# Kernel tuning notes

Hardware: AMD Instinct MI355X
Metric: run time of the kernel (lower is better)

## Reference

```python
import jax, jax.numpy as jnp
import numpy as np

N_NODES = 50000
N_EDGES = 1600000
NODE_DIM = 16
EDGE_DIM = 16
PIPE_F = 4
HID = 64
L = 3


def _lin(k, fan_in, fan_out):
    kw, kb = jax.random.split(k)
    bound = 1.0 / np.sqrt(fan_in)
    w = jax.random.uniform(kw, (fan_in, fan_out), jnp.float32, -bound, bound)
    b = jax.random.uniform(kb, (fan_out,), jnp.float32, -bound, bound)
    return w, b


def setup_inputs() -> dict:
    key = jax.random.key(0)
    ks = jax.random.split(key, 16)
    leak_area = jax.random.normal(ks[0], (N_NODES, 1), jnp.float32)
    pipe_attrs = jax.random.normal(ks[1], (N_EDGES, PIPE_F), jnp.float32)
    edge_index = jax.random.randint(ks[2], (2, N_EDGES), 0, N_NODES, jnp.int32)
    node_embed_w, node_embed_b = _lin(ks[3], 1, NODE_DIM)
    edge_embed_w, edge_embed_b = _lin(ks[4], PIPE_F, EDGE_DIM)
    # per-layer MLP params, stacked along leading layer axis
    ew1, eb1, ew2, eb2, nw1, nb1, nw2, nb2 = [], [], [], [], [], [], [], []
    for l in range(L):
        kl = jax.random.fold_in(ks[5], l)
        k1, k2, k3, k4 = jax.random.split(kl, 4)
        w, b = _lin(k1, 2 * NODE_DIM + EDGE_DIM, HID); ew1.append(w); eb1.append(b)
        w, b = _lin(k2, HID, EDGE_DIM); ew2.append(w); eb2.append(b)
        w, b = _lin(k3, NODE_DIM + EDGE_DIM, HID); nw1.append(w); nb1.append(b)
        w, b = _lin(k4, HID, NODE_DIM); nw2.append(w); nb2.append(b)
    final_node_w, final_node_b = _lin(ks[6], NODE_DIM, 1)
    final_edge_w, final_edge_b = _lin(ks[7], EDGE_DIM, 1)
    return {
        "leak_area": leak_area,
        "pipe_attrs": pipe_attrs,
        "edge_index": edge_index,
        "node_embed_w": node_embed_w, "node_embed_b": node_embed_b,
        "edge_embed_w": edge_embed_w, "edge_embed_b": edge_embed_b,
        "edge_mlp_w1": jnp.stack(ew1), "edge_mlp_b1": jnp.stack(eb1),
        "edge_mlp_w2": jnp.stack(ew2), "edge_mlp_b2": jnp.stack(eb2),
        "node_mlp_w1": jnp.stack(nw1), "node_mlp_b1": jnp.stack(nb1),
        "node_mlp_w2": jnp.stack(nw2), "node_mlp_b2": jnp.stack(nb2),
        "final_node_w": final_node_w, "final_node_b": final_node_b,
        "final_edge_w": final_edge_w, "final_edge_b": final_edge_b,
    }


def reference(leak_area, pipe_attrs, edge_index,
              node_embed_w, node_embed_b, edge_embed_w, edge_embed_b,
              edge_mlp_w1, edge_mlp_b1, edge_mlp_w2, edge_mlp_b2,
              node_mlp_w1, node_mlp_b1, node_mlp_w2, node_mlp_b2,
              final_node_w, final_node_b, final_edge_w, final_edge_b):
    x = leak_area @ node_embed_w + node_embed_b          # [N, node_dim]
    e = pipe_attrs @ edge_embed_w + edge_embed_b          # [E, edge_dim]
    src = edge_index[0]  # x_j (source, PyG default flow source_to_target)
    dst = edge_index[1]  # x_i (target); aggregation index
    n = x.shape[0]
    num_layers = edge_mlp_w1.shape[0]
    ones = jnp.ones((src.shape[0], 1), x.dtype)
    deg = jax.ops.segment_sum(ones, dst, num_segments=n)  # [N,1]
    inv_deg = 1.0 / jnp.maximum(deg, 1.0)
    for l in range(num_layers):
        # message: small MLP on [x_i, x_j, e] per edge
        m_in = jnp.concatenate([x[dst], x[src], e], axis=-1)       # [E, 2d+de]
        h = jax.nn.relu(m_in @ edge_mlp_w1[l] + edge_mlp_b1[l])    # [E, 64]
        msg = h @ edge_mlp_w2[l] + edge_mlp_b2[l]                  # [E, de]
        # mean-aggregate to target nodes
        aggr = jax.ops.segment_sum(msg, dst, num_segments=n) * inv_deg  # [N, de]
        # node update MLP
        u_in = jnp.concatenate([x, aggr], axis=-1)                 # [N, d+de]
        x = jax.nn.relu(u_in @ node_mlp_w1[l] + node_mlp_b1[l]) @ node_mlp_w2[l] + node_mlp_b2[l]
    H = (x @ final_node_w + final_node_b)[:, 0]   # [N]
    q = (e @ final_edge_w + final_edge_b)[:, 0]   # [E]
    return H, q
```

## Files before the change

kernel.cpp:

```cpp
#include <hip/hip_runtime.h>
#include <hip/hip_bf16.h>

#define NN 50000
#define NE 1600000
#define NB 391
#define CBLK 392
#define EPB 4096

typedef __attribute__((ext_vector_type(8))) short bf16x8;
typedef __attribute__((ext_vector_type(4))) float f32x4;

#define B_HAG   0
#define B_QW    (B_HAG + NN*64*4)
#define B_NF    (B_QW + 32)
#define B_W1B   (B_NF + 3*8*64*8*2)
#define B_XB0   (B_W1B + 3*8*64*8*2)
#define B_XB1   (B_XB0 + NN*16*2)
#define B_EPK   (B_XB1 + NN*16*2)
#define B_OFF   (B_EPK + NE*16)
#define B_BCNT  (B_OFF + (NN+1)*4)
#define B_BASE  (B_BCNT + CBLK*NB*4)
#define B_END   (B_BASE + (NB+1)*4)

static __device__ __forceinline__ unsigned short f2bf(float f) {
    union { __hip_bfloat16 h; unsigned short u; } cv;
    cv.h = __float2bfloat16(f);
    return cv.u;
}
static __device__ __forceinline__ unsigned pk2(float a, float b) {
    unsigned r;
    asm("v_cvt_pk_bf16_f32 %0, %1, %2" : "=v"(r) : "v"(a), "v"(b));
    return r;
}
static __device__ __forceinline__ float bf2f(unsigned short u) {
    return __uint_as_float((unsigned)u << 16);
}
static __device__ __forceinline__ bf16x8 mk8(unsigned a, unsigned b, unsigned c, unsigned d) {
    union { bf16x8 v; uint4 u; } cv;
    cv.u = make_uint4(a, b, c, d);
    return cv.v;
}

__global__ void prep_kernel(const float* __restrict__ ew1, const float* __restrict__ eb1,
                            const float* __restrict__ nw1, const float* __restrict__ ew2,
                            const float* __restrict__ nw2,
                            const float* __restrict__ eeW, const float* __restrict__ eeB,
                            const float* __restrict__ few, const float* __restrict__ feb,
                            unsigned short* __restrict__ w1b, unsigned short* __restrict__ nf,
                            float* __restrict__ qw)
{
    int t0 = blockIdx.x * blockDim.x + threadIdx.x;
    int stride = gridDim.x * blockDim.x;
    for (int idx = t0; idx < 3 * 8 * 64 * 8; idx += stride) {
        int l = idx >> 12;
        int r = idx & 4095;
        int f = r >> 9;
        int lane = (r >> 3) & 63;
        int e = r & 7;
        int col = lane & 15;
        int krow = ((lane >> 4) << 3) + e;
        {
            int tt = f >> 1, s = f & 1;
            int k = krow + (s << 5);
            int j = (tt << 4) + col;
            float v = 0.f;
            if (k < 32) {
                v = ew1[l * 3072 + k * 64 + j];
            } else if (k < 36) {
                int f2 = k - 32;
                float acc = 0.f;
                for (int m = 0; m < 16; m++) acc += eeW[f2 * 16 + m] * ew1[l * 3072 + (32 + m) * 64 + j];
                v = acc;
            } else if (k == 36) {
                float acc = eb1[l * 64 + j];
                for (int m = 0; m < 16; m++) acc += eeB[m] * ew1[l * 3072 + (32 + m) * 64 + j];
                v = acc;
            }
            w1b[idx] = f2bf(v);
        }
        {
            float v;
            if (f < 2)      v = ew2[l * 1024 + (f * 32 + krow) * 16 + col];
            else if (f < 6) v = nw1[l * 2048 + krow * 64 + (f - 2) * 16 + col];
            else            v = nw2[l * 1024 + ((f - 6) * 32 + krow) * 16 + col];
            nf[idx] = f2bf(v);
        }
    }
    if (t0 < 4) {
        float s = 0.f;
        for (int k = 0; k < 16; k++) s += eeW[t0 * 16 + k] * few[k];
        qw[t0] = s;
    } else if (t0 == 4) {
        float s = feb[0];
        for (int k = 0; k < 16; k++) s += eeB[k] * few[k];
        qw[4] = s;
    }
}

__global__ __launch_bounds__(256) void node_init_kernel(
    const float* __restrict__ leak, const float* __restrict__ nw, const float* __restrict__ nb,
    unsigned short* __restrict__ xb0, float* __restrict__ hag)
{
    int n = blockIdx.x * blockDim.x + threadIdx.x;
    if (n >= NN) return;
    float la = leak[n];
    float v[16];
    #pragma unroll
    for (int i = 0; i < 16; i++) v[i] = la * nw[i] + nb[i];
    unsigned pk[8];
    #pragma unroll
    for (int i = 0; i < 8; i++) pk[i] = pk2(v[2 * i], v[2 * i + 1]);
    uint4* xo = reinterpret_cast<uint4*>(xb0 + n * 16);
    xo[0] = make_uint4(pk[0], pk[1], pk[2], pk[3]);
    xo[1] = make_uint4(pk[4], pk[5], pk[6], pk[7]);
    float4 z = {0.f, 0.f, 0.f, 0.f};
    float4* hp = reinterpret_cast<float4*>(hag + n * 64);
    #pragma unroll
    for (int j = 0; j < 16; j++) hp[j] = z;
}

__global__ __launch_bounds__(1024) void bucket_count_kernel(
    const int* __restrict__ dst, int* __restrict__ bcnt)
{
    __shared__ int hist[NB];
    int t = threadIdx.x;
    for (int i = t; i < NB; i += 1024) hist[i] = 0;
    __syncthreads();
    int base = blockIdx.x * EPB;
    #pragma unroll
    for (int i = 0; i < 4; i++) {
        int idx = base + i * 1024 + t;
        if (idx < NE) atomicAdd(&hist[dst[idx] >> 7], 1);
    }
    __syncthreads();
    for (int i = t; i < NB; i += 1024) bcnt[blockIdx.x * NB + i] = hist[i];
}

__global__ __launch_bounds__(512) void bucket_scan_kernel(
    int* __restrict__ bcnt, int* __restrict__ gbase)
{
    __shared__ int sm[512];
    int t = threadIdx.x;
    int tot = 0;
    if (t < NB)
        for (int blk = 0; blk < CBLK; blk++) tot += bcnt[blk * NB + t];
    sm[t] = tot;
    __syncthreads();
    for (int o = 1; o < 512; o <<= 1) {
        int v = (t >= o) ? sm[t - o] : 0;
        __syncthreads();
        sm[t] += v;
        __syncthreads();
    }
    int excl = sm[t] - tot;
    if (t < NB) {
        gbase[t] = excl;
        int run = excl;
        for (int blk = 0; blk < CBLK; blk++) {
            int c = bcnt[blk * NB + t];
            bcnt[blk * NB + t] = run;
            run += c;
        }
    }
    if (t == 0) gbase[NB] = NE;
}

__global__ __launch_bounds__(1024) void bucket_scatter_kernel(
    const int* __restrict__ ei, const float* __restrict__ pa,
    const int* __restrict__ bcnt, const float* __restrict__ qw,
    float* __restrict__ qout, uint4* __restrict__ epk)
{
    __shared__ int hist[NB];
    int t = threadIdx.x;
    for (int i = t; i < NB; i += 1024) hist[i] = 0;
    __syncthreads();
    int base = blockIdx.x * EPB;
    #pragma unroll
    for (int i = 0; i < 4; i++) {
        int idx = base + i * 1024 + t;
        if (idx < NE) {
            int d = ei[NE + idx];
            int b = d >> 7;
            float4 p = reinterpret_cast<const float4*>(pa)[idx];
            qout[idx] = qw[4] + p.x * qw[0] + p.y * qw[1] + p.z * qw[2] + p.w * qw[3];
            int lr = atomicAdd(&hist[b], 1);
            int pos = bcnt[blockIdx.x * NB + b] + lr;
            uint4 v;
            v.x = (unsigned)ei[idx];
            v.y = (unsigned)d;
            v.z = pk2(p.x, p.y);
            v.w = pk2(p.z, p.w);
            epk[pos] = v;
        }
    }
}

__global__ __launch_bounds__(1024) void fine_sort_kernel(
    const int* __restrict__ gbase, uint4* __restrict__ epk, int* __restrict__ off)
{
    __shared__ int hist[128];
    __shared__ int fb[128];
    int t = threadIdx.x;
    int b = blockIdx.x;
    int S = gbase[b], E = gbase[b + 1];
    if (t < 128) hist[t] = 0;
    __syncthreads();

    uint4 r[12];
    int lr[12];
    #pragma unroll
    for (int i = 0; i < 12; i++) {
        int gi = S + i * 1024 + t;
        if (gi < E) {
            r[i] = epk[gi];
            lr[i] = atomicAdd(&hist[(int)(r[i].y & 127u)], 1);
        }
    }
    __syncthreads();
    if (t < 128) fb[t] = hist[t];
    __syncthreads();
    for (int o = 1; o < 128; o <<= 1) {
        int v = 0;
        if (t < 128 && t >= o) v = fb[t - o];
        __syncthreads();
        if (t < 128) fb[t] += v;
        __syncthreads();
    }
    int d0 = b << 7;
    if (t < 128 && d0 + t < NN) off[d0 + t] = S + fb[t] - hist[t];
    if (b == NB - 1 && t == 0) off[NN] = NE;
    __syncthreads();
    #pragma unroll
    for (int i = 0; i < 12; i++) {
        int gi = S + i * 1024 + t;
        if (gi < E) {
            int fd = (int)(r[i].y & 127u);
            int pos = S + (fb[fd] - hist[fd]) + lr[i];
            epk[pos] = r[i];
        }
    }
}

__global__ __launch_bounds__(256, 4) void edge_mfma_kernel(
    const unsigned short* __restrict__ xb,
    const uint4* __restrict__ epk,
    const int* __restrict__ off,
    const unsigned short* __restrict__ w1b,
    float* __restrict__ hag)
{
    __shared__ unsigned short hbuf[4][64 * 68];
    int tid = threadIdx.x;
    int lane = tid & 63;
    int wid = tid >> 6;
    int wave = blockIdx.x * 4 + wid;
    int base = wave * 64;
    if (base >= NE) return;
    int ar = lane & 15;
    int ap = lane >> 4;
    unsigned short* hb = &hbuf[wid][0];

    uint4 ev0 = epk[base + 0  + ar];
    uint4 ev1 = epk[base + 16 + ar];
    uint4 ev2 = epk[base + 32 + ar];
    uint4 ev3 = epk[base + 48 + ar];

    int r0 = (ap < 2) ? (int)ev0.y : (int)ev0.x;
    int r1 = (ap < 2) ? (int)ev1.y : (int)ev1.x;
    int r2 = (ap < 2) ? (int)ev2.y : (int)ev2.x;
    int r3 = (ap < 2) ? (int)ev3.y : (int)ev3.x;
    int half = (ap & 1) * 8;
    bf16x8 a00 = *reinterpret_cast<const bf16x8*>(xb + (size_t)r0 * 16 + half);
    bf16x8 a01 = *reinterpret_cast<const bf16x8*>(xb + (size_t)r1 * 16 + half);
    bf16x8 a02 = *reinterpret_cast<const bf16x8*>(xb + (size_t)r2 * 16 + half);
    bf16x8 a03 = *reinterpret_cast<const bf16x8*>(xb + (size_t)r3 * 16 + half);

    int d0 = __builtin_amdgcn_readfirstlane((int)ev0.y);

    bf16x8 Bf[8];
    const bf16x8* w1v = reinterpret_cast<const bf16x8*>(w1b);
    #pragma unroll
    for (int i = 0; i < 8; i++) Bf[i] = w1v[i * 64 + lane];

#define DO_TILE(EV, A0, TILE) do {                                             \
    bf16x8 a1 = (bf16x8)0;                                                     \
    if (ap == 0) {                                                             \
        a1[0] = (short)(EV.z & 0xffffu);                                       \
        a1[1] = (short)(EV.z >> 16);                                           \
        a1[2] = (short)(EV.w & 0xffffu);                                       \
        a1[3] = (short)(EV.w >> 16);                                           \
        a1[4] = (short)0x3f80;                                                 \
    }                                                                          \
    f32x4 C0 = {0.f, 0.f, 0.f, 0.f}, C1 = C0, C2 = C0, C3 = C0;                \
    C0 = __builtin_amdgcn_mfma_f32_16x16x32_bf16(A0, Bf[0], C0, 0, 0, 0);      \
    C0 = __builtin_amdgcn_mfma_f32_16x16x32_bf16(a1, Bf[1], C0, 0, 0, 0);      \
    C1 = __builtin_amdgcn_mfma_f32_16x16x32_bf16(A0, Bf[2], C1, 0, 0, 0);      \
    C1 = __builtin_amdgcn_mfma_f32_16x16x32_bf16(a1, Bf[3], C1, 0, 0, 0);      \
    C2 = __builtin_amdgcn_mfma_f32_16x16x32_bf16(A0, Bf[4], C2, 0, 0, 0);      \
    C2 = __builtin_amdgcn_mfma_f32_16x16x32_bf16(a1, Bf[5], C2, 0, 0, 0);      \
    C3 = __builtin_amdgcn_mfma_f32_16x16x32_bf16(A0, Bf[6], C3, 0, 0, 0);      \
    C3 = __builtin_amdgcn_mfma_f32_16x16x32_bf16(a1, Bf[7], C3, 0, 0, 0);      \
    int eoff = TILE * 16 + ap * 4;                                             \
    {                                                                          \
        unsigned lov = pk2(fmaxf(C0[0], 0.f), fmaxf(C0[1], 0.f));              \
        unsigned hiv = pk2(fmaxf(C0[2], 0.f), fmaxf(C0[3], 0.f));              \
        *reinterpret_cast<uint2*>(hb + (0 * 16 + ar) * 68 + eoff) = make_uint2(lov, hiv); \
    }                                                                          \
    {                                                                          \
        unsigned lov = pk2(fmaxf(C1[0], 0.f), fmaxf(C1[1], 0.f));              \
        unsigned hiv = pk2(fmaxf(C1[2], 0.f), fmaxf(C1[3], 0.f));              \
        *reinterpret_cast<uint2*>(hb + (1 * 16 + ar) * 68 + eoff) = make_uint2(lov, hiv); \
    }                                                                          \
    {                                                                          \
        unsigned lov = pk2(fmaxf(C2[0], 0.f), fmaxf(C2[1], 0.f));              \
        unsigned hiv = pk2(fmaxf(C2[2], 0.f), fmaxf(C2[3], 0.f));              \
        *reinterpret_cast<uint2*>(hb + (2 * 16 + ar) * 68 + eoff) = make_uint2(lov, hiv); \
    }                                                                          \
    {                                                                          \
        unsigned lov = pk2(fmaxf(C3[0], 0.f), fmaxf(C3[1], 0.f));              \
        unsigned hiv = pk2(fmaxf(C3[2], 0.f), fmaxf(C3[3], 0.f));              \
        *reinterpret_cast<uint2*>(hb + (3 * 16 + ar) * 68 + eoff) = make_uint2(lov, hiv); \
    }                                                                          \
} while (0)

    DO_TILE(ev0, a00, 0);
    DO_TILE(ev1, a01, 1);
    DO_TILE(ev2, a02, 2);
    DO_TILE(ev3, a03, 3);
#undef DO_TILE

    asm volatile("s_waitcnt lgkmcnt(0)" ::: "memory");
    __builtin_amdgcn_sched_barrier(0);

    int d = d0;
    int e = base;
    const int lim = base + 64;
    const unsigned short* hr = hb + lane * 68;
    while (e < lim) {
        int segend = off[d + 1];
        int eend = segend < lim ? segend : lim;
        float acc = 0.f;
        int i = e - base, iend = eend - base;
        for (; (i & 3) != 0 && i < iend; ++i) acc += bf2f(hr[i]);
        for (; i + 4 <= iend; i += 4) {
            uint2 u = *reinterpret_cast<const uint2*>(hr + i);
            acc += __uint_as_float(u.x << 16) + __uint_as_float(u.x & 0xffff0000u)
                 + __uint_as_float(u.y << 16) + __uint_as_float(u.y & 0xffff0000u);
        }
        for (; i < iend; ++i) acc += bf2f(hr[i]);
        unsafeAtomicAdd(&hag[(size_t)d * 64 + lane], acc);
        e = eend;
        if (segend <= lim) ++d;
    }
}

__global__ __launch_bounds__(256) void node_mfma_kernel(
    const unsigned short* __restrict__ xb, unsigned short* __restrict__ xbn,
    float* __restrict__ hag, const int* __restrict__ off,
    const unsigned short* __restrict__ nf,
    const float* __restrict__ eb2,
    const float* __restrict__ nb1, const float* __restrict__ nb2,
    const float* __restrict__ fnw, const float* __restrict__ fnb,
    float* __restrict__ Hout, int writeH)
{
    __shared__ unsigned short aggt[4][16 * 16];
    __shared__ unsigned short ht[4][16 * 64];
    __shared__ float ot[4][16 * 16];
    int tid = threadIdx.x;
    int lane = tid & 63;
    int wid = tid >> 6;
    int wave = blockIdx.x * 4 + wid;
    int n0 = wave * 16;
    if (n0 >= NN) return;
    int nr = lane & 15;
    int ap = lane >> 4;

    bf16x8 Bf[8];
    const bf16x8* nfv = reinterpret_cast<const bf16x8*>(nf);
    #pragma unroll
    for (int i = 0; i < 8; i++) Bf[i] = nfv[i * 64 + lane];

    float* hrow = hag + (size_t)(n0 + nr) * 64 + ap * 8;
    float4* h0p = reinterpret_cast<float4*>(hrow);
    float4* h1p = reinterpret_cast<float4*>(hrow + 32);
    float4 ha = h0p[0], hc = h0p[1];
    float4 he = h1p[0], hg = h1p[1];
    float4 z = {0.f, 0.f, 0.f, 0.f};
    h0p[0] = z; h0p[1] = z; h1p[0] = z; h1p[1] = z;
    bf16x8 agA0 = mk8(pk2(ha.x, ha.y), pk2(ha.z, ha.w), pk2(hc.x, hc.y), pk2(hc.z, hc.w));
    bf16x8 agA1 = mk8(pk2(he.x, he.y), pk2(he.z, he.w), pk2(hg.x, hg.y), pk2(hg.z, hg.w));
    f32x4 Cag = {0.f, 0.f, 0.f, 0.f};
    Cag = __builtin_amdgcn_mfma_f32_16x16x32_bf16(agA0, Bf[0], Cag, 0, 0, 0);
    Cag = __builtin_amdgcn_mfma_f32_16x16x32_bf16(agA1, Bf[1], Cag, 0, 0, 0);

    int bn = n0 + ap * 4;
    int o0 = off[bn], o1 = off[bn + 1], o2 = off[bn + 2], o3 = off[bn + 3], o4 = off[bn + 4];
    float ebv = eb2[nr];
    {
        int dgs[4] = {o1 - o0, o2 - o1, o3 - o2, o4 - o3};
        #pragma unroll
        for (int r = 0; r < 4; r++) {
            float inv = 1.0f / (float)(dgs[r] > 0 ? dgs[r] : 1);
            float val = Cag[r] * inv + ((dgs[r] > 0) ? ebv : 0.f);
            aggt[wid][(ap * 4 + r) * 16 + nr] = f2bf(val);
        }
    }
    asm volatile("s_waitcnt lgkmcnt(0)" ::: "memory");
    __builtin_amdgcn_sched_barrier(0);

    bf16x8 uA;
    if (ap < 2) uA = *reinterpret_cast<const bf16x8*>(xb + (size_t)(n0 + nr) * 16 + ap * 8);
    else        uA = *reinterpret_cast<const bf16x8*>(&aggt[wid][nr * 16 + (ap - 2) * 8]);

    f32x4 Ch0 = {0.f, 0.f, 0.f, 0.f}, Ch1 = Ch0, Ch2 = Ch0, Ch3 = Ch0;
    Ch0 = __builtin_amdgcn_mfma_f32_16x16x32_bf16(uA, Bf[2], Ch0, 0, 0, 0);
    Ch1 = __builtin_amdgcn_mfma_f32_16x16x32_bf16(uA, Bf[3], Ch1, 0, 0, 0);
    Ch2 = __builtin_amdgcn_mfma_f32_16x16x32_bf16(uA, Bf[4], Ch2, 0, 0, 0);
    Ch3 = __builtin_amdgcn_mfma_f32_16x16x32_bf16(uA, Bf[5], Ch3, 0, 0, 0);

#define H_EPI(C, TT) do {                                                      \
    int j = (TT) * 16 + nr;                                                    \
    float bv = nb1[j];                                                         \
    _Pragma("unroll")                                                          \
    for (int r = 0; r < 4; r++) {                                              \
        float h = fmaxf(C[r] + bv, 0.f);                                       \
        ht[wid][(ap * 4 + r) * 64 + j] = f2bf(h);                              \
    }                                                                          \
} while (0)
    H_EPI(Ch0, 0); H_EPI(Ch1, 1); H_EPI(Ch2, 2); H_EPI(Ch3, 3);
#undef H_EPI

    asm volatile("s_waitcnt lgkmcnt(0)" ::: "memory");
    __builtin_amdgcn_sched_barrier(0);

    bf16x8 hA0 = *reinterpret_cast<const bf16x8*>(&ht[wid][nr * 64 + ap * 8]);
    bf16x8 hA1 = *reinterpret_cast<const bf16x8*>(&ht[wid][nr * 64 + 32 + ap * 8]);
    f32x4 Co = {0.f, 0.f, 0.f, 0.f};
    Co = __builtin_amdgcn_mfma_f32_16x16x32_bf16(hA0, Bf[6], Co, 0, 0, 0);
    Co = __builtin_amdgcn_mfma_f32_16x16x32_bf16(hA1, Bf[7], Co, 0, 0, 0);
    {
        float bv = nb2[nr];
        #pragma unroll
        for (int r = 0; r < 4; r++) ot[wid][(ap * 4 + r) * 16 + nr] = Co[r] + bv;
    }
    asm volatile("s_waitcnt lgkmcnt(0)" ::: "memory");
    __builtin_amdgcn_sched_barrier(0);

    if (lane < 16) {
        const float* orow = &ot[wid][lane * 16];
        float o[16];
        #pragma unroll
        for (int k = 0; k < 16; k++) o[k] = orow[k];
        unsigned pk[8];
        #pragma unroll
        for (int i = 0; i < 8; i++) pk[i] = pk2(o[2 * i], o[2 * i + 1]);
        uint4* xo = reinterpret_cast<uint4*>(xbn + (size_t)(n0 + lane) * 16);
        xo[0] = make_uint4(pk[0], pk[1], pk[2], pk[3]);
        xo[1] = make_uint4(pk[4], pk[5], pk[6], pk[7]);
        if (writeH) {
            float s = fnb[0];
            #pragma unroll
            for (int k = 0; k < 16; k++) s += o[k] * fnw[k];
            Hout[n0 + lane] = s;
        }
    }
}

extern "C" void kernel_launch(void* const* d_in, const int* in_sizes, int n_in,
                              void* d_out, int out_size, void* d_ws, size_t ws_size,
                              hipStream_t stream)
{
    const float* leak = (const float*)d_in[0];
    const float* pa   = (const float*)d_in[1];
    const int*   ei   = (const int*)d_in[2];
    const float* neww = (const float*)d_in[3];
    const float* newb = (const float*)d_in[4];
    const float* eeW  = (const float*)d_in[5];
    const float* eeB  = (const float*)d_in[6];
    const float* ew1  = (const float*)d_in[7];
    const float* eb1  = (const float*)d_in[8];
    const float* ew2  = (const float*)d_in[9];
    const float* eb2  = (const float*)d_in[10];
    const float* nw1  = (const float*)d_in[11];
    const float* nb1  = (const float*)d_in[12];
    const float* nw2  = (const float*)d_in[13];
    const float* nb2  = (const float*)d_in[14];
    const float* fnw  = (const float*)d_in[15];
    const float* fnb  = (const float*)d_in[16];
    const float* few  = (const float*)d_in[17];
    const float* feb  = (const float*)d_in[18];

    char* wsb = (char*)d_ws;
    float*          hag   = (float*)(wsb + B_HAG);
    float*          qw    = (float*)(wsb + B_QW);
    unsigned short* nf    = (unsigned short*)(wsb + B_NF);
    unsigned short* w1b   = (unsigned short*)(wsb + B_W1B);
    unsigned short* xb0   = (unsigned short*)(wsb + B_XB0);
    unsigned short* xb1   = (unsigned short*)(wsb + B_XB1);
    uint4*          epk   = (uint4*)(wsb + B_EPK);
    int*            off   = (int*)(wsb + B_OFF);
    int*            bcnt  = (int*)(wsb + B_BCNT);
    int*            gbase = (int*)(wsb + B_BASE);

    float* H = (float*)d_out;
    float* q = (float*)d_out + NN;
    const int* dstp = ei + NE;

    prep_kernel<<<16, 256, 0, stream>>>(ew1, eb1, nw1, ew2, nw2, eeW, eeB, few, feb,
                                        w1b, nf, qw);
    node_init_kernel<<<(NN + 255) / 256, 256, 0, stream>>>(leak, neww, newb, xb0, hag);
    bucket_count_kernel<<<CBLK, 1024, 0, stream>>>(dstp, bcnt);
    bucket_scan_kernel<<<1, 512, 0, stream>>>(bcnt, gbase);
    bucket_scatter_kernel<<<CBLK, 1024, 0, stream>>>(ei, pa, bcnt, qw, q, epk);
    fine_sort_kernel<<<NB, 1024, 0, stream>>>(gbase, epk, off);

    int nwaves = NN / 16;
    int nblocks = (nwaves + 3) / 4;

    unsigned short* xcur = xb0;
    unsigned short* xnxt = xb1;
    for (int l = 0; l < 3; l++) {
        edge_mfma_kernel<<<NE / 256, 256, 0, stream>>>(
            xcur, epk, off, w1b + l * 4096, hag);
        node_mfma_kernel<<<nblocks, 256, 0, stream>>>(
            xcur, xnxt, hag, off, nf + l * 4096, eb2 + l * 16,
            nb1 + l * 64, nb2 + l * 16, fnw, fnb, H, (l == 2) ? 1 : 0);
        unsigned short* tmp = xcur; xcur = xnxt; xnxt = tmp;
    }
}
```

Before: 229.7 us.

## Parallelize bucket prefix scan across blocks and shrink edge kernel blocks

```diff
diff --git a/kernel.cpp b/kernel.cpp
--- a/kernel.cpp
+++ b/kernel.cpp
@@ -20,7 +20,8 @@
 #define B_OFF   (B_EPK + NE*16)
 #define B_BCNT  (B_OFF + (NN+1)*4)
 #define B_BASE  (B_BCNT + CBLK*NB*4)
-#define B_END   (B_BASE + (NB+1)*4)
+#define B_GTOT  (B_BASE + (NB+1)*4)
+#define B_END   (B_GTOT + NB*4)
 
 static __device__ __forceinline__ unsigned short f2bf(float f) {
     union { __hip_bfloat16 h; unsigned short u; } cv;
@@ -136,38 +137,47 @@
     for (int i = t; i < NB; i += 1024) bcnt[blockIdx.x * NB + i] = hist[i];
 }
 
-__global__ __launch_bounds__(512) void bucket_scan_kernel(
-    int* __restrict__ bcnt, int* __restrict__ gbase)
+__global__ __launch_bounds__(512) void scan_blocks_kernel(
+    int* __restrict__ bcnt, int* __restrict__ gtot)
+{
+    __shared__ int sm[512];
+    int b = blockIdx.x;
+    int t = threadIdx.x;
+    int v = (t < CBLK) ? bcnt[t * NB + b] : 0;
+    sm[t] = v;
+    __syncthreads();
+    for (int o = 1; o < 512; o <<= 1) {
+        int x = (t >= o) ? sm[t - o] : 0;
+        __syncthreads();
+        sm[t] += x;
+        __syncthreads();
+    }
+    if (t < CBLK) bcnt[t * NB + b] = sm[t] - v;
+    if (t == 511) gtot[b] = sm[511];
+}
+
+__global__ __launch_bounds__(512) void scan_top_kernel(
+    const int* __restrict__ gtot, int* __restrict__ gbase)
 {
     __shared__ int sm[512];
     int t = threadIdx.x;
-    int tot = 0;
-    if (t < NB)
-        for (int blk = 0; blk < CBLK; blk++) tot += bcnt[blk * NB + t];
-    sm[t] = tot;
+    int v = (t < NB) ? gtot[t] : 0;
+    sm[t] = v;
     __syncthreads();
     for (int o = 1; o < 512; o <<= 1) {
-        int v = (t >= o) ? sm[t - o] : 0;
+        int x = (t >= o) ? sm[t - o] : 0;
         __syncthreads();
-        sm[t] += v;
+        sm[t] += x;
         __syncthreads();
     }
-    int excl = sm[t] - tot;
-    if (t < NB) {
-        gbase[t] = excl;
-        int run = excl;
-        for (int blk = 0; blk < CBLK; blk++) {
-            int c = bcnt[blk * NB + t];
-            bcnt[blk * NB + t] = run;
-            run += c;
-        }
-    }
+    if (t < NB) gbase[t] = sm[t] - v;
     if (t == 0) gbase[NB] = NE;
 }
 
 __global__ __launch_bounds__(1024) void bucket_scatter_kernel(
     const int* __restrict__ ei, const float* __restrict__ pa,
-    const int* __restrict__ bcnt, const float* __restrict__ qw,
+    const int* __restrict__ bcnt, const int* __restrict__ gbase,
+    const float* __restrict__ qw,
     float* __restrict__ qout, uint4* __restrict__ epk)
 {
     __shared__ int hist[NB];
@@ -184,7 +194,7 @@
             float4 p = reinterpret_cast<const float4*>(pa)[idx];
             qout[idx] = qw[4] + p.x * qw[0] + p.y * qw[1] + p.z * qw[2] + p.w * qw[3];
             int lr = atomicAdd(&hist[b], 1);
-            int pos = bcnt[blockIdx.x * NB + b] + lr;
+            int pos = gbase[b] + bcnt[blockIdx.x * NB + b] + lr;
             uint4 v;
             v.x = (unsigned)ei[idx];
             v.y = (unsigned)d;
@@ -241,18 +251,18 @@
     }
 }
 
-__global__ __launch_bounds__(256, 4) void edge_mfma_kernel(
+__global__ __launch_bounds__(128, 5) void edge_mfma_kernel(
     const unsigned short* __restrict__ xb,
     const uint4* __restrict__ epk,
     const int* __restrict__ off,
     const unsigned short* __restrict__ w1b,
     float* __restrict__ hag)
 {
-    __shared__ unsigned short hbuf[4][64 * 68];
+    __shared__ unsigned short hbuf[2][64 * 68];
     int tid = threadIdx.x;
     int lane = tid & 63;
     int wid = tid >> 6;
-    int wave = blockIdx.x * 4 + wid;
+    int wave = blockIdx.x * 2 + wid;
     int base = wave * 64;
     if (base >= NE) return;
     int ar = lane & 15;
@@ -500,6 +510,7 @@
     int*            off   = (int*)(wsb + B_OFF);
     int*            bcnt  = (int*)(wsb + B_BCNT);
     int*            gbase = (int*)(wsb + B_BASE);
+    int*            gtot  = (int*)(wsb + B_GTOT);
 
     float* H = (float*)d_out;
     float* q = (float*)d_out + NN;
@@ -509,8 +520,9 @@
                                         w1b, nf, qw);
     node_init_kernel<<<(NN + 255) / 256, 256, 0, stream>>>(leak, neww, newb, xb0, hag);
     bucket_count_kernel<<<CBLK, 1024, 0, stream>>>(dstp, bcnt);
-    bucket_scan_kernel<<<1, 512, 0, stream>>>(bcnt, gbase);
-    bucket_scatter_kernel<<<CBLK, 1024, 0, stream>>>(ei, pa, bcnt, qw, q, epk);
+    scan_blocks_kernel<<<NB, 512, 0, stream>>>(bcnt, gtot);
+    scan_top_kernel<<<1, 512, 0, stream>>>(gtot, gbase);
+    bucket_scatter_kernel<<<CBLK, 1024, 0, stream>>>(ei, pa, bcnt, gbase, qw, q, epk);
     fine_sort_kernel<<<NB, 1024, 0, stream>>>(gbase, epk, off);
 
     int nwaves = NN / 16;
@@ -519,7 +531,7 @@
     unsigned short* xcur = xb0;
     unsigned short* xnxt = xb1;
     for (int l = 0; l < 3; l++) {
-        edge_mfma_kernel<<<NE / 256, 256, 0, stream>>>(
+        edge_mfma_kernel<<<NE / 128, 128, 0, stream>>>(
             xcur, epk, off, w1b + l * 4096, hag);
         node_mfma_kernel<<<nblocks, 256, 0, stream>>>(
             xcur, xnxt, hag, off, nf + l * 4096, eb2 + l * 16,
```

Result: faster. 200.7 us (-12.6%).
